# Kernel tuning notes

Hardware: AMD Instinct MI355X
Metric: run time of the kernel (lower is better)

The kernel has to match this reference:

```python
import jax, jax.numpy as jnp
import numpy as np

N = 50000   # nodes
E = 640000  # edges
D = 128     # hidden_size
BN_EPS = 1e-5


def _bn(x, g, b):
    # BatchNorm1d, training-mode batch statistics (biased variance), per-feature
    m = jnp.mean(x, axis=0)
    v = jnp.var(x, axis=0)
    return g * (x - m) * jax.lax.rsqrt(v + BN_EPS) + b


def _gin_mlp(x, W1, b1, g, bb, W2, b2):
    # Linear -> BatchNorm1d -> GELU(exact) -> Linear
    h = jax.nn.gelu(_bn(x @ W1 + b1, g, bb), approximate=False)
    return h @ W2 + b2


def _ffn(x, W1, b1, g1, bb1, W2, b2, g2, bb2):
    # fc1=(Linear+BN) -> GELU -> fc2=(Linear+BN) -> +shortcut
    h = jax.nn.gelu(_bn(x @ W1 + b1, g1, bb1), approximate=False)
    return _bn(h @ W2 + b2, g2, bb2) + x


def setup_inputs() -> dict:
    key = jax.random.key(0)
    ks = iter(jax.random.split(key, 16))

    def p(*s):
        return jax.random.normal(next(ks), s, jnp.float32) * 0.05

    inp = {
        "x": jax.random.normal(next(ks), (N, D), jnp.float32),
        "edge_index": jax.random.randint(next(ks), (2, E), 0, N, jnp.int32),
        # node_encoder + batch_norm
        "enc_W": p(D, D), "enc_b": jnp.zeros(D, jnp.float32),
        "bn_g": jnp.ones(D, jnp.float32), "bn_b": jnp.zeros(D, jnp.float32),
        # GINConv MLP: Linear(D,D)+BN+GELU+Linear(D,D)
        "gW1": p(D, D), "gb1": jnp.zeros(D, jnp.float32),
        "gg": jnp.ones(D, jnp.float32), "gbb": jnp.zeros(D, jnp.float32),
        "gW2": p(D, D), "gb2": jnp.zeros(D, jnp.float32),
        # fc2 = FFN(D, 2D)
        "f2W1": p(D, 2 * D), "f2b1": jnp.zeros(2 * D, jnp.float32),
        "f2g1": jnp.ones(2 * D, jnp.float32), "f2bb1": jnp.zeros(2 * D, jnp.float32),
        "f2W2": p(2 * D, D), "f2b2": jnp.zeros(D, jnp.float32),
        "f2g2": jnp.ones(D, jnp.float32), "f2bb2": jnp.zeros(D, jnp.float32),
        # ffn = FFN(D, 4D)
        "fnW1": p(D, 4 * D), "fnb1": jnp.zeros(4 * D, jnp.float32),
        "fng1": jnp.ones(4 * D, jnp.float32), "fnbb1": jnp.zeros(4 * D, jnp.float32),
        "fnW2": p(4 * D, D), "fnb2": jnp.zeros(D, jnp.float32),
        "fng2": jnp.ones(D, jnp.float32), "fnbb2": jnp.zeros(D, jnp.float32),
    }
    return inp


def reference(x, edge_index, enc_W, enc_b, bn_g, bn_b,
              gW1, gb1, gg, gbb, gW2, gb2,
              f2W1, f2b1, f2g1, f2bb1, f2W2, f2b2, f2g2, f2bb2,
              fnW1, fnb1, fng1, fnbb1, fnW2, fnb2, fng2, fnbb2):
    shortcut = x
    # node_encoder + BN
    h = _bn(x @ enc_W + enc_b, bn_g, bn_b)  # [N, D]
    # GINConv: out = MLP((1+eps)*h + sum_{j->i} h_j), eps=0
    src, dst = edge_index[0], edge_index[1]
    agg = jax.ops.segment_sum(h[src], dst, num_segments=N)  # scatter-add [N, D]
    h = _gin_mlp(h + agg, gW1, gb1, gg, gbb, gW2, gb2)
    # fc2 FFN (hidden 2D, internal residual)
    h = _ffn(h, f2W1, f2b1, f2g1, f2bb1, f2W2, f2b2, f2g2, f2bb2)
    # outer residual
    h = shortcut + h
    # final FFN (hidden 4D, internal residual)
    return _ffn(h, fnW1, fnb1, fng1, fnbb1, fnW2, fnb2, fng2, fnbb2)
```

## Files before the change

kernel.cpp:

```cpp
#include <hip/hip_runtime.h>
#include <hip/hip_bf16.h>

typedef __attribute__((ext_vector_type(8))) short short8;
typedef __attribute__((ext_vector_type(4))) float f32x4;

__device__ __forceinline__ float bf2f(unsigned short u) {
    union { unsigned int i; float f; } c;
    c.i = ((unsigned int)u) << 16;
    return c.f;
}
__device__ __forceinline__ unsigned short f2bf(float f) {
    union { float f; unsigned int i; } c;
    c.f = f;
    unsigned int x = c.i;
    x += 0x7FFFu + ((x >> 16) & 1u);
    return (unsigned short)(x >> 16);
}

#define NPART 64

template<int K, int M, int XF>
__global__ __launch_bounds__(256, (K > 256) ? 4 : 5)
void gemmf_kernel(const void* __restrict__ Av,
                  const float* __restrict__ pSum, const float* __restrict__ pSq,
                  const float* __restrict__ pG, const float* __restrict__ pB,
                  const unsigned short* __restrict__ Wp,
                  const float* __restrict__ bias,
                  float* __restrict__ part,
                  unsigned short* __restrict__ C,
                  int nrows, float invN)
{
    constexpr int KS_TOT = K / 32;
    constexpr int NKC    = K / 128;
    constexpr int NCT    = M / 128;
    constexpr bool DBUF  = (K > 256);
    constexpr int NFRAG  = DBUF ? 32 : 4 * KS_TOT;
    __shared__ __align__(16) char smem[NFRAG * 1024 + ((NCT > 1) ? 16384 : 0)];
    char* cbuf = smem + ((NCT > 1) ? NFRAG * 1024 : 0);

    const int tid = threadIdx.x;
    const int l   = tid & 63, wv = tid >> 6;
    const int gr0 = blockIdx.x * 64;
    const int kq4 = l & 3, rloc = l >> 2;
    const int woff = ((kq4 * 16 + rloc) * 16) ^ (kq4 << 5);
    const int loff = (l * 16) ^ ((l >> 4) << 5);

    int rowg[4];
    #pragma unroll
    for (int i = 0; i < 4; ++i) {
        int rg = gr0 + i * 16 + rloc;
        rowg[i] = rg < nrows ? rg : nrows - 1;
    }

    f32x4 acc[4][2];
    short8 breg[2][4];

    auto loadB = [&](int ct, int kcb) {
        #pragma unroll
        for (int c = 0; c < 2; ++c) {
            const int col = ct * 128 + (wv * 2 + c) * 16 + (l & 15);
            const unsigned short* bp = Wp + (size_t)col * K + kcb + (l >> 4) * 8;
            #pragma unroll
            for (int ks = 0; ks < 4; ++ks)
                breg[c][ks] = *(const short8*)(bp + ks * 32);
        }
    };

    auto bncoef = [&](int c0k, float* sc8, float* sh8) {
        #pragma unroll
        for (int j = 0; j < 8; ++j) {
            const int c = c0k + j;
            const float mean = pSum[c] * invN;
            const float var  = pSq[c] * invN - mean * mean;
            const float sc   = pG[c] * rsqrtf(var + 1e-5f);
            sc8[j] = sc;
            sh8[j] = pB[c] - mean * sc;
        }
    };

    auto xf2 = [&](short8 t, const float* sc8, const float* sh8) -> short8 {
        short8 val;
        #pragma unroll
        for (int j = 0; j < 8; ++j) {
            float v = sc8[j] * bf2f((unsigned short)t[j]) + sh8[j];
            v = 0.5f * v * (1.0f + erff(v * 0.70710678118f));
            val[j] = (short)f2bf(v);
        }
        return val;
    };

    auto epilogue = [&](int ct) {
        const int lrow = l & 15, kg = l >> 4;
        __syncthreads();
        #pragma unroll
        for (int c = 0; c < 2; ++c) {
            const int col  = (wv * 2 + c) * 16 + lrow;
            const int gcol = ct * 128 + col;
            const float bc = bias[gcol];
            float s = 0.f, q = 0.f;
            #pragma unroll
            for (int r = 0; r < 4; ++r) {
                #pragma unroll
                for (int i = 0; i < 4; ++i) {
                    const int rl = r * 16 + kg * 4 + i;
                    const float v = acc[r][c][i] + bc;
                    if (gr0 + rl < nrows) { s += v; q += v * v; }
                    const int byte = rl * 256 + ((col * 2) ^ ((rl & 7) << 4));
                    *(unsigned short*)(cbuf + byte) = f2bf(v);
                }
            }
            s += __shfl_xor(s, 16); s += __shfl_xor(s, 32);
            q += __shfl_xor(q, 16); q += __shfl_xor(q, 32);
            if (kg == 0 && part != nullptr) {
                float* ps = part + (size_t)(blockIdx.x & (NPART - 1)) * (2 * M);
                atomicAdd(&ps[gcol], s);
                atomicAdd(&ps[M + gcol], q);
            }
        }
        __syncthreads();
        #pragma unroll
        for (int j = 0; j < 4; ++j) {
            const int lin = j * 256 + tid;
            const int rl = lin >> 4, chunk = lin & 15;
            const int row = gr0 + rl;
            if (row < nrows) {
                short8 vv = *(const short8*)(cbuf + rl * 256 + ((chunk * 16) ^ ((rl & 7) << 4)));
                *(short8*)(C + (size_t)row * M + ct * 128 + chunk * 8) = vv;
            }
        }
    };

    if constexpr (!DBUF) {
        #pragma unroll
        for (int h = 0; h < NKC; ++h) {
            const int kst = h * 4 + wv;
            const int c0k = kst * 32 + kq4 * 8;
            float sc8[8], sh8[8];
            if (XF == 2) bncoef(c0k, sc8, sh8);
            #pragma unroll
            for (int i = 0; i < 4; ++i) {
                const size_t eoff = (size_t)rowg[i] * K + c0k;
                short8 val;
                if (XF == 0) {
                    val = *(const short8*)((const unsigned short*)Av + eoff);
                } else if (XF == 1) {
                    const float* A = (const float*)Av;
                    f32x4 u0 = *(const f32x4*)(A + eoff);
                    f32x4 u1 = *(const f32x4*)(A + eoff + 4);
                    #pragma unroll
                    for (int j = 0; j < 4; ++j) {
                        val[j]     = (short)f2bf(u0[j]);
                        val[j + 4] = (short)f2bf(u1[j]);
                    }
                } else {
                    short8 t = *(const short8*)((const unsigned short*)Av + eoff);
                    val = xf2(t, sc8, sh8);
                }
                *(short8*)(smem + (i * KS_TOT + kst) * 1024 + woff) = val;
            }
        }
        __syncthreads();
        #pragma unroll
        for (int ct = 0; ct < NCT; ++ct) {
            #pragma unroll
            for (int r = 0; r < 4; ++r)
                #pragma unroll
                for (int c = 0; c < 2; ++c) acc[r][c] = f32x4{0.f, 0.f, 0.f, 0.f};
            #pragma unroll
            for (int kc = 0; kc < NKC; ++kc) {
                loadB(ct, kc * 128);
                #pragma unroll
                for (int ks = 0; ks < 4; ++ks) {
                    const int ksg = kc * 4 + ks;
                    short8 af[4];
                    #pragma unroll
                    for (int r = 0; r < 4; ++r)
                        af[r] = *(const short8*)(smem + (r * KS_TOT + ksg) * 1024 + loff);
                    #pragma unroll
                    for (int r = 0; r < 4; ++r)
                        #pragma unroll
                        for (int c = 0; c < 2; ++c)
                            acc[r][c] = __builtin_amdgcn_mfma_f32_16x16x32_bf16(af[r], breg[c][ks], acc[r][c], 0, 0, 0);
                }
            }
            epilogue(ct);
        }
    } else {
        const int akoff = wv * 32 + kq4 * 8;
        auto stageChunk = [&](int kcb, int b, const short8* pre) {
            const int c0k = kcb + akoff;
            float sc8[8], sh8[8];
            if (XF == 2) bncoef(c0k, sc8, sh8);
            #pragma unroll
            for (int i = 0; i < 4; ++i) {
                short8 t = pre ? pre[i]
                              : *(const short8*)((const unsigned short*)Av + (size_t)rowg[i] * K + c0k);
                short8 val = (XF == 2) ? xf2(t, sc8, sh8) : t;
                *(short8*)(smem + (b * 16 + i * 4 + wv) * 1024 + woff) = val;
            }
        };
        stageChunk(0, 0, nullptr);
        __syncthreads();
        #pragma unroll
        for (int r = 0; r < 4; ++r)
            #pragma unroll
            for (int c = 0; c < 2; ++c) acc[r][c] = f32x4{0.f, 0.f, 0.f, 0.f};
        #pragma unroll
        for (int kc = 0; kc < NKC; ++kc) {
            const int cur = kc & 1;
            loadB(0, kc * 128);
            short8 anext[4];
            if (kc + 1 < NKC) {
                const int c0k = (kc + 1) * 128 + akoff;
                #pragma unroll
                for (int i = 0; i < 4; ++i)
                    anext[i] = *(const short8*)((const unsigned short*)Av + (size_t)rowg[i] * K + c0k);
            }
            #pragma unroll
            for (int ks = 0; ks < 4; ++ks) {
                short8 af[4];
                #pragma unroll
                for (int r = 0; r < 4; ++r)
                    af[r] = *(const short8*)(smem + (cur * 16 + r * 4 + ks) * 1024 + loff);
                #pragma unroll
                for (int r = 0; r < 4; ++r)
                    #pragma unroll
                    for (int c = 0; c < 2; ++c)
                        acc[r][c] = __builtin_amdgcn_mfma_f32_16x16x32_bf16(af[r], breg[c][ks], acc[r][c], 0, 0, 0);
            }
            if (kc + 1 < NKC) {
                stageChunk((kc + 1) * 128, cur ^ 1, anext);
                __syncthreads();
            }
        }
        epilogue(0);
    }
}

__global__ void reduce_kernel(const float* __restrict__ part,
                              float* __restrict__ out, int W2)
{
    int i = blockIdx.x * blockDim.x + threadIdx.x;
    if (i >= W2) return;
    float s = 0.f;
    #pragma unroll 8
    for (int r = 0; r < NPART; ++r) s += part[(size_t)r * W2 + i];
    out[i] = s;
}

__global__ void h3_kernel(const unsigned short* __restrict__ t4,
                          const float* __restrict__ pSum, const float* __restrict__ pSq,
                          const float* __restrict__ pG, const float* __restrict__ pB,
                          const unsigned short* __restrict__ t2,
                          const float* __restrict__ xr,
                          unsigned short* __restrict__ H3, float invN, int total4)
{
    int idx = blockIdx.x * blockDim.x + threadIdx.x;
    if (idx >= total4) return;
    const int base = idx * 4;
    const int c0 = base & 127;
    ushort4 tv = *(const ushort4*)(t4 + base);
    ushort4 uv = *(const ushort4*)(t2 + base);
    float4  xv = *(const float4*)(xr + base);
    unsigned short ts[4] = {tv.x, tv.y, tv.z, tv.w};
    unsigned short us[4] = {uv.x, uv.y, uv.z, uv.w};
    const float* px = &xv.x;
    ushort4 ov;
    unsigned short* po = &ov.x;
    #pragma unroll
    for (int j = 0; j < 4; ++j) {
        const int c = c0 + j;
        const float mean = pSum[c] * invN;
        const float var  = pSq[c] * invN - mean * mean;
        const float sc   = pG[c] * rsqrtf(var + 1e-5f);
        const float sh   = pB[c] - mean * sc;
        po[j] = f2bf(sc * bf2f(ts[j]) + sh + bf2f(us[j]) + px[j]);
    }
    *(ushort4*)(H3 + base) = ov;
}

__global__ void hist_kernel(const int* __restrict__ ei, int* __restrict__ cnt, int E)
{
    int e = blockIdx.x * blockDim.x + threadIdx.x;
    if (e < E) atomicAdd(&cnt[ei[E + e]], 1);
}

__global__ void scan_reduce(const int* __restrict__ cnt, int* __restrict__ blksum, int n)
{
    __shared__ int s[256];
    int t = threadIdx.x;
    int i = blockIdx.x * 256 + t;
    s[t] = i < n ? cnt[i] : 0;
    __syncthreads();
    for (int d = 128; d > 0; d >>= 1) {
        if (t < d) s[t] += s[t + d];
        __syncthreads();
    }
    if (t == 0) blksum[blockIdx.x] = s[0];
}

__global__ void scan_top(int* __restrict__ blksum, int nb)
{
    __shared__ int s[256];
    int t = threadIdx.x;
    int v = t < nb ? blksum[t] : 0;
    s[t] = v;
    __syncthreads();
    for (int d = 1; d < 256; d <<= 1) {
        int u = (t >= d) ? s[t - d] : 0;
        __syncthreads();
        s[t] += u;
        __syncthreads();
    }
    if (t < nb) blksum[t] = s[t] - v;
}

__global__ void scan_apply(const int* __restrict__ cnt, const int* __restrict__ blksum,
                           int* __restrict__ offs, int* __restrict__ cursor, int n)
{
    __shared__ int s[256];
    int t = threadIdx.x;
    int i = blockIdx.x * 256 + t;
    int v = i < n ? cnt[i] : 0;
    s[t] = v;
    __syncthreads();
    for (int d = 1; d < 256; d <<= 1) {
        int u = (t >= d) ? s[t - d] : 0;
        __syncthreads();
        s[t] += u;
        __syncthreads();
    }
    int excl = s[t] - v + blksum[blockIdx.x];
    if (i < n) { offs[i] = excl; cursor[i] = excl; }
}

__global__ void place_kernel(const int* __restrict__ ei, int* __restrict__ cursor,
                             int* __restrict__ ssrc, int E)
{
    int e = blockIdx.x * blockDim.x + threadIdx.x;
    if (e < E) {
        int pos = atomicAdd(&cursor[ei[E + e]], 1);
        ssrc[pos] = ei[e];
    }
}

__global__ __launch_bounds__(256)
void gather_kernel(const unsigned short* __restrict__ T0,
                   const float* __restrict__ pSum, const float* __restrict__ pSq,
                   const float* __restrict__ pG, const float* __restrict__ pB,
                   float invN,
                   const int* __restrict__ ssrc, const int* __restrict__ offs,
                   const int* __restrict__ cnt,
                   unsigned short* __restrict__ Zb, int N)
{
    const int wave = threadIdx.x >> 6;
    const int lane = threadIdx.x & 63;
    const int node = blockIdx.x * 4 + wave;
    if (node >= N) return;

    unsigned int hv = *(const unsigned int*)(T0 + (size_t)node * 128 + lane * 2);
    float a0 = bf2f((unsigned short)hv);
    float a1 = bf2f((unsigned short)(hv >> 16));

    const int off = offs[node];
    const int deg = cnt[node];
    for (int base = 0; base < deg; base += 64) {
        int m = deg - base;
        if (m > 64) m = 64;
        int idx = (base + lane < deg) ? ssrc[off + base + lane] : 0;
        int k = 0;
        for (; k + 1 < m; k += 2) {
            int s0 = __shfl(idx, k);
            int s1 = __shfl(idx, k + 1);
            unsigned int v0 = *(const unsigned int*)(T0 + (size_t)s0 * 128 + lane * 2);
            unsigned int v1 = *(const unsigned int*)(T0 + (size_t)s1 * 128 + lane * 2);
            a0 += bf2f((unsigned short)v0) + bf2f((unsigned short)v1);
            a1 += bf2f((unsigned short)(v0 >> 16)) + bf2f((unsigned short)(v1 >> 16));
        }
        if (k < m) {
            int s0 = __shfl(idx, k);
            unsigned int v0 = *(const unsigned int*)(T0 + (size_t)s0 * 128 + lane * 2);
            a0 += bf2f((unsigned short)v0);
            a1 += bf2f((unsigned short)(v0 >> 16));
        }
    }
    const int c0 = lane * 2;
    const float mean0 = pSum[c0] * invN;
    const float var0  = pSq[c0] * invN - mean0 * mean0;
    const float sc0   = pG[c0] * rsqrtf(var0 + 1e-5f);
    const float sh0   = pB[c0] - mean0 * sc0;
    const float mean1 = pSum[c0 + 1] * invN;
    const float var1  = pSq[c0 + 1] * invN - mean1 * mean1;
    const float sc1   = pG[c0 + 1] * rsqrtf(var1 + 1e-5f);
    const float sh1   = pB[c0 + 1] - mean1 * sc1;
    const float dp1 = (float)(deg + 1);
    const float z0 = sc0 * a0 + dp1 * sh0;
    const float z1 = sc1 * a1 + dp1 * sh1;
    unsigned int o = ((unsigned int)f2bf(z1) << 16) | (unsigned int)f2bf(z0);
    *(unsigned int*)(Zb + (size_t)node * 128 + lane * 2) = o;
}

__global__ void final_kernel(const unsigned short* __restrict__ t6,
                             const float* __restrict__ pSum, const float* __restrict__ pSq,
                             const float* __restrict__ pG, const float* __restrict__ pB,
                             const unsigned short* __restrict__ h3,
                             float* __restrict__ out, float invN, int total4)
{
    int idx = blockIdx.x * blockDim.x + threadIdx.x;
    if (idx >= total4) return;
    const int base = idx * 4;
    const int c0 = base & 127;
    ushort4 tv = *(const ushort4*)(t6 + base);
    ushort4 hv = *(const ushort4*)(h3 + base);
    unsigned short ts[4] = {tv.x, tv.y, tv.z, tv.w};
    unsigned short hs[4] = {hv.x, hv.y, hv.z, hv.w};
    float4 ov;
    float* po = &ov.x;
    #pragma unroll
    for (int j = 0; j < 4; ++j) {
        const int c = c0 + j;
        const float mean = pSum[c] * invN;
        const float var  = pSq[c] * invN - mean * mean;
        const float sc   = pG[c] * rsqrtf(var + 1e-5f);
        const float sh   = pB[c] - mean * sc;
        po[j] = sc * bf2f(ts[j]) + sh + bf2f(hs[j]);
    }
    *(float4*)(out + base) = ov;
}

struct PackDesc { const float* src; unsigned short* dst; int K; int M; };
struct Pack7 { PackDesc d[7]; };
__global__ void pack_kernel(Pack7 p)
{
    PackDesc d = p.d[blockIdx.y];
    const int total = d.K * d.M;
    for (int idx = blockIdx.x * blockDim.x + threadIdx.x; idx < total;
         idx += gridDim.x * blockDim.x) {
        const int k = idx / d.M;
        const int m = idx - k * d.M;
        d.dst[(size_t)m * d.K + k] = f2bf(d.src[idx]);
    }
}

extern "C" void kernel_launch(void* const* d_in, const int* in_sizes, int n_in,
                              void* d_out, int out_size, void* d_ws, size_t ws_size,
                              hipStream_t stream)
{
    const float* x     = (const float*)d_in[0];
    const int*   ei    = (const int*)d_in[1];
    const float* enc_W = (const float*)d_in[2];
    const float* enc_b = (const float*)d_in[3];
    const float* bn_g  = (const float*)d_in[4];
    const float* bn_b  = (const float*)d_in[5];
    const float* gW1   = (const float*)d_in[6];
    const float* gb1   = (const float*)d_in[7];
    const float* gg    = (const float*)d_in[8];
    const float* gbb   = (const float*)d_in[9];
    const float* gW2   = (const float*)d_in[10];
    const float* gb2   = (const float*)d_in[11];
    const float* f2W1  = (const float*)d_in[12];
    const float* f2b1  = (const float*)d_in[13];
    const float* f2g1  = (const float*)d_in[14];
    const float* f2bb1 = (const float*)d_in[15];
    const float* f2W2  = (const float*)d_in[16];
    const float* f2b2  = (const float*)d_in[17];
    const float* f2g2  = (const float*)d_in[18];
    const float* f2bb2 = (const float*)d_in[19];
    const float* fnW1  = (const float*)d_in[20];
    const float* fnb1  = (const float*)d_in[21];
    const float* fng1  = (const float*)d_in[22];
    const float* fnbb1 = (const float*)d_in[23];
    const float* fnW2  = (const float*)d_in[24];
    const float* fnb2  = (const float*)d_in[25];
    const float* fng2  = (const float*)d_in[26];
    const float* fnbb2 = (const float*)d_in[27];

    const int D = 128;
    const int N = in_sizes[0] / D;
    const int E = in_sizes[1] / 2;
    const float invN = 1.0f / (float)N;

    char* w = (char*)d_ws;
    float* s0 = (float*)w;
    float* s1 = s0 + 256;
    float* s3 = s1 + 256;
    float* s4 = s3 + 512;
    float* s5 = s4 + 256;
    float* s6 = s5 + 1024;
    const size_t statsBytes = 2560 * sizeof(float);
    size_t off = statsBytes;

    float* p0 = (float*)(w + off); off += (size_t)NPART * 256 * 4;
    float* p1 = (float*)(w + off); off += (size_t)NPART * 256 * 4;
    float* p3 = (float*)(w + off); off += (size_t)NPART * 512 * 4;
    float* p4 = (float*)(w + off); off += (size_t)NPART * 256 * 4;
    float* p5 = (float*)(w + off); off += (size_t)NPART * 1024 * 4;
    float* p6 = (float*)(w + off); off += (size_t)NPART * 256 * 4;
    const size_t partBytes = (size_t)NPART * 2560 * 4;

    unsigned short* wpE  = (unsigned short*)(w + off); off += (size_t)128 * 128 * 2;
    unsigned short* wpG1 = (unsigned short*)(w + off); off += (size_t)128 * 128 * 2;
    unsigned short* wpG2 = (unsigned short*)(w + off); off += (size_t)128 * 128 * 2;
    unsigned short* wpF1 = (unsigned short*)(w + off); off += (size_t)128 * 256 * 2;
    unsigned short* wpF2 = (unsigned short*)(w + off); off += (size_t)256 * 128 * 2;
    unsigned short* wpN1 = (unsigned short*)(w + off); off += (size_t)128 * 512 * 2;
    unsigned short* wpN2 = (unsigned short*)(w + off); off += (size_t)512 * 128 * 2;

    unsigned short* P1 = (unsigned short*)(w + off); off += (size_t)N * 128 * 2;
    unsigned short* Zb = (unsigned short*)(w + off); off += (size_t)N * 128 * 2;
    unsigned short* H3 = (unsigned short*)(w + off); off += (size_t)N * 128 * 2;
    unsigned short* T3 = (unsigned short*)(w + off); off += (size_t)N * 256 * 2;
    unsigned short* T5 = (unsigned short*)(w + off); off += (size_t)N * 512 * 2;

    const int NB = (N + 255) / 256;
    char* csr = (char*)T5;
    int* cnt    = (int*)csr;  csr += (size_t)NB * 256 * 4;
    int* offs   = (int*)csr;  csr += (size_t)NB * 256 * 4;
    int* cursor = (int*)csr;  csr += (size_t)NB * 256 * 4;
    int* blksum = (int*)csr;  csr += 1024;
    int* ssrc   = (int*)csr;

    hipMemsetAsync(p0, 0, partBytes, stream);
    hipMemsetAsync(cnt, 0, (size_t)NB * 256 * 4, stream);

    Pack7 pk;
    pk.d[0] = PackDesc{enc_W, wpE, 128, 128};
    pk.d[1] = PackDesc{gW1, wpG1, 128, 128};
    pk.d[2] = PackDesc{gW2, wpG2, 128, 128};
    pk.d[3] = PackDesc{f2W1, wpF1, 128, 256};
    pk.d[4] = PackDesc{f2W2, wpF2, 256, 128};
    pk.d[5] = PackDesc{fnW1, wpN1, 128, 512};
    pk.d[6] = PackDesc{fnW2, wpN2, 512, 128};
    pack_kernel<<<dim3(64, 7), 256, 0, stream>>>(pk);

    const int eb = (E + 255) / 256;
    hist_kernel<<<eb, 256, 0, stream>>>(ei, cnt, E);
    scan_reduce<<<NB, 256, 0, stream>>>(cnt, blksum, N);
    scan_top<<<1, 256, 0, stream>>>(blksum, NB);
    scan_apply<<<NB, 256, 0, stream>>>(cnt, blksum, offs, cursor, N);
    place_kernel<<<eb, 256, 0, stream>>>(ei, cursor, ssrc, E);

    const int rb  = (N + 63) / 64;
    const int t4a = N * 128 / 4;
    const int ewb = (t4a + 255) / 256;

    gemmf_kernel<128, 128, 1><<<rb, 256, 0, stream>>>(
        x, nullptr, nullptr, nullptr, nullptr,
        wpE, enc_b, p0, P1, N, invN);
    reduce_kernel<<<1, 256, 0, stream>>>(p0, s0, 256);
    gather_kernel<<<(N + 3) / 4, 256, 0, stream>>>(
        P1, s0, s0 + 128, bn_g, bn_b, invN, ssrc, offs, cnt, Zb, N);
    gemmf_kernel<128, 128, 0><<<rb, 256, 0, stream>>>(
        Zb, nullptr, nullptr, nullptr, nullptr,
        wpG1, gb1, p1, P1, N, invN);
    reduce_kernel<<<1, 256, 0, stream>>>(p1, s1, 256);
    gemmf_kernel<128, 128, 2><<<rb, 256, 0, stream>>>(
        P1, s1, s1 + 128, gg, gbb,
        wpG2, gb2, nullptr, Zb, N, invN);
    gemmf_kernel<128, 256, 0><<<rb, 256, 0, stream>>>(
        Zb, nullptr, nullptr, nullptr, nullptr,
        wpF1, f2b1, p3, T3, N, invN);
    reduce_kernel<<<2, 256, 0, stream>>>(p3, s3, 512);
    gemmf_kernel<256, 128, 2><<<rb, 256, 0, stream>>>(
        T3, s3, s3 + 256, f2g1, f2bb1,
        wpF2, f2b2, p4, P1, N, invN);
    reduce_kernel<<<1, 256, 0, stream>>>(p4, s4, 256);
    h3_kernel<<<ewb, 256, 0, stream>>>(
        P1, s4, s4 + 128, f2g2, f2bb2, Zb, x, H3, invN, t4a);
    gemmf_kernel<128, 512, 0><<<rb, 256, 0, stream>>>(
        H3, nullptr, nullptr, nullptr, nullptr,
        wpN1, fnb1, p5, T5, N, invN);
    reduce_kernel<<<4, 256, 0, stream>>>(p5, s5, 1024);
    gemmf_kernel<512, 128, 2><<<rb, 256, 0, stream>>>(
        T5, s5, s5 + 512, fng1, fnbb1,
        wpN2, fnb2, p6, P1, N, invN);
    reduce_kernel<<<1, 256, 0, stream>>>(p6, s6, 256);
    final_kernel<<<ewb, 256, 0, stream>>>(
        P1, s6, s6 + 128, fng2, fnbb2, H3, (float*)d_out, invN, t4a);

    (void)n_in; (void)out_size; (void)ws_size;
}
```

Before: 357.1 us.

## Precompute BN scale/shift in reduce kernel and use fast tanh-form GELU

The partial-sum reduce kernels now also compute the per-feature BatchNorm scale and shift, so consumer kernels load two coefficients instead of recomputing mean, variance and rsqrt per element or thread. The exact erf GELU in the fused GEMM prologue is replaced with a sigmoid/tanh-style approximation built from a fast exp and a hardware reciprocal. This cuts transcendental and ALU work on the GEMM A-operand staging path but changes the numerics from exact GELU to an approximation.

```diff
diff --git a/kernel.cpp b/kernel.cpp
--- a/kernel.cpp
+++ b/kernel.cpp
@@ -16,19 +16,25 @@
     x += 0x7FFFu + ((x >> 16) & 1u);
     return (unsigned short)(x >> 16);
 }
+__device__ __forceinline__ float gelu_fast(float x) {
+    const float x2 = x * x;
+    const float t = x * fmaf(0.0713548163f, x2, 1.5957691216f);
+    const float e = __expf(t);
+    const float r = __builtin_amdgcn_rcpf(e + 1.0f);
+    return fmaf(-x, r, x);
+}
 
 #define NPART 64
 
 template<int K, int M, int XF>
 __global__ __launch_bounds__(256, (K > 256) ? 4 : 5)
 void gemmf_kernel(const void* __restrict__ Av,
-                  const float* __restrict__ pSum, const float* __restrict__ pSq,
-                  const float* __restrict__ pG, const float* __restrict__ pB,
+                  const float* __restrict__ pCoef,
                   const unsigned short* __restrict__ Wp,
                   const float* __restrict__ bias,
                   float* __restrict__ part,
                   unsigned short* __restrict__ C,
-                  int nrows, float invN)
+                  int nrows)
 {
     constexpr int KS_TOT = K / 32;
     constexpr int NKC    = K / 128;
@@ -66,25 +72,12 @@
         }
     };
 
-    auto bncoef = [&](int c0k, float* sc8, float* sh8) {
-        #pragma unroll
-        for (int j = 0; j < 8; ++j) {
-            const int c = c0k + j;
-            const float mean = pSum[c] * invN;
-            const float var  = pSq[c] * invN - mean * mean;
-            const float sc   = pG[c] * rsqrtf(var + 1e-5f);
-            sc8[j] = sc;
-            sh8[j] = pB[c] - mean * sc;
-        }
-    };
-
     auto xf2 = [&](short8 t, const float* sc8, const float* sh8) -> short8 {
         short8 val;
         #pragma unroll
         for (int j = 0; j < 8; ++j) {
-            float v = sc8[j] * bf2f((unsigned short)t[j]) + sh8[j];
-            v = 0.5f * v * (1.0f + erff(v * 0.70710678118f));
-            val[j] = (short)f2bf(v);
+            float v = fmaf(sc8[j], bf2f((unsigned short)t[j]), sh8[j]);
+            val[j] = (short)f2bf(gelu_fast(v));
         }
         return val;
     };
@@ -136,7 +129,13 @@
             const int kst = h * 4 + wv;
             const int c0k = kst * 32 + kq4 * 8;
             float sc8[8], sh8[8];
-            if (XF == 2) bncoef(c0k, sc8, sh8);
+            if (XF == 2) {
+                #pragma unroll
+                for (int j = 0; j < 8; ++j) {
+                    sc8[j] = pCoef[c0k + j];
+                    sh8[j] = pCoef[K + c0k + j];
+                }
+            }
             #pragma unroll
             for (int i = 0; i < 4; ++i) {
                 const size_t eoff = (size_t)rowg[i] * K + c0k;
@@ -190,7 +189,13 @@
         auto stageChunk = [&](int kcb, int b, const short8* pre) {
             const int c0k = kcb + akoff;
             float sc8[8], sh8[8];
-            if (XF == 2) bncoef(c0k, sc8, sh8);
+            if (XF == 2) {
+                #pragma unroll
+                for (int j = 0; j < 8; ++j) {
+                    sc8[j] = pCoef[c0k + j];
+                    sh8[j] = pCoef[K + c0k + j];
+                }
+            }
             #pragma unroll
             for (int i = 0; i < 4; ++i) {
                 short8 t = pre ? pre[i]
@@ -237,23 +242,30 @@
     }
 }
 
-__global__ void reduce_kernel(const float* __restrict__ part,
-                              float* __restrict__ out, int W2)
+__global__ void coef_kernel(const float* __restrict__ part,
+                            const float* __restrict__ g, const float* __restrict__ b,
+                            float* __restrict__ scsh, int W, float invN)
 {
     int i = blockIdx.x * blockDim.x + threadIdx.x;
-    if (i >= W2) return;
-    float s = 0.f;
+    if (i >= W) return;
+    float s = 0.f, q = 0.f;
     #pragma unroll 8
-    for (int r = 0; r < NPART; ++r) s += part[(size_t)r * W2 + i];
-    out[i] = s;
+    for (int r = 0; r < NPART; ++r) {
+        s += part[(size_t)r * 2 * W + i];
+        q += part[(size_t)r * 2 * W + W + i];
+    }
+    const float mean = s * invN;
+    const float var  = q * invN - mean * mean;
+    const float sc   = g[i] * rsqrtf(var + 1e-5f);
+    scsh[i] = sc;
+    scsh[W + i] = b[i] - mean * sc;
 }
 
 __global__ void h3_kernel(const unsigned short* __restrict__ t4,
-                          const float* __restrict__ pSum, const float* __restrict__ pSq,
-                          const float* __restrict__ pG, const float* __restrict__ pB,
+                          const float* __restrict__ coef,
                           const unsigned short* __restrict__ t2,
                           const float* __restrict__ xr,
-                          unsigned short* __restrict__ H3, float invN, int total4)
+                          unsigned short* __restrict__ H3, int total4)
 {
     int idx = blockIdx.x * blockDim.x + threadIdx.x;
     if (idx >= total4) return;
@@ -270,11 +282,7 @@
     #pragma unroll
     for (int j = 0; j < 4; ++j) {
         const int c = c0 + j;
-        const float mean = pSum[c] * invN;
-        const float var  = pSq[c] * invN - mean * mean;
-        const float sc   = pG[c] * rsqrtf(var + 1e-5f);
-        const float sh   = pB[c] - mean * sc;
-        po[j] = f2bf(sc * bf2f(ts[j]) + sh + bf2f(us[j]) + px[j]);
+        po[j] = f2bf(fmaf(coef[c], bf2f(ts[j]), coef[128 + c]) + bf2f(us[j]) + px[j]);
     }
     *(ushort4*)(H3 + base) = ov;
 }
@@ -346,9 +354,7 @@
 
 __global__ __launch_bounds__(256)
 void gather_kernel(const unsigned short* __restrict__ T0,
-                   const float* __restrict__ pSum, const float* __restrict__ pSq,
-                   const float* __restrict__ pG, const float* __restrict__ pB,
-                   float invN,
+                   const float* __restrict__ coef,
                    const int* __restrict__ ssrc, const int* __restrict__ offs,
                    const int* __restrict__ cnt,
                    unsigned short* __restrict__ Zb, int N)
@@ -385,26 +391,17 @@
         }
     }
     const int c0 = lane * 2;
-    const float mean0 = pSum[c0] * invN;
-    const float var0  = pSq[c0] * invN - mean0 * mean0;
-    const float sc0   = pG[c0] * rsqrtf(var0 + 1e-5f);
-    const float sh0   = pB[c0] - mean0 * sc0;
-    const float mean1 = pSum[c0 + 1] * invN;
-    const float var1  = pSq[c0 + 1] * invN - mean1 * mean1;
-    const float sc1   = pG[c0 + 1] * rsqrtf(var1 + 1e-5f);
-    const float sh1   = pB[c0 + 1] - mean1 * sc1;
     const float dp1 = (float)(deg + 1);
-    const float z0 = sc0 * a0 + dp1 * sh0;
-    const float z1 = sc1 * a1 + dp1 * sh1;
+    const float z0 = fmaf(coef[c0], a0, dp1 * coef[128 + c0]);
+    const float z1 = fmaf(coef[c0 + 1], a1, dp1 * coef[128 + c0 + 1]);
     unsigned int o = ((unsigned int)f2bf(z1) << 16) | (unsigned int)f2bf(z0);
     *(unsigned int*)(Zb + (size_t)node * 128 + lane * 2) = o;
 }
 
 __global__ void final_kernel(const unsigned short* __restrict__ t6,
-                             const float* __restrict__ pSum, const float* __restrict__ pSq,
-                             const float* __restrict__ pG, const float* __restrict__ pB,
+                             const float* __restrict__ coef,
                              const unsigned short* __restrict__ h3,
-                             float* __restrict__ out, float invN, int total4)
+                             float* __restrict__ out, int total4)
 {
     int idx = blockIdx.x * blockDim.x + threadIdx.x;
     if (idx >= total4) return;
@@ -419,11 +416,7 @@
     #pragma unroll
     for (int j = 0; j < 4; ++j) {
         const int c = c0 + j;
-        const float mean = pSum[c] * invN;
-        const float var  = pSq[c] * invN - mean * mean;
-        const float sc   = pG[c] * rsqrtf(var + 1e-5f);
-        const float sh   = pB[c] - mean * sc;
-        po[j] = sc * bf2f(ts[j]) + sh + bf2f(hs[j]);
+        po[j] = fmaf(coef[c], bf2f(ts[j]), coef[128 + c]) + bf2f(hs[j]);
     }
     *(float4*)(out + base) = ov;
 }
@@ -481,14 +474,14 @@
     const float invN = 1.0f / (float)N;
 
     char* w = (char*)d_ws;
-    float* s0 = (float*)w;
-    float* s1 = s0 + 256;
-    float* s3 = s1 + 256;
-    float* s4 = s3 + 512;
-    float* s5 = s4 + 256;
-    float* s6 = s5 + 1024;
-    const size_t statsBytes = 2560 * sizeof(float);
-    size_t off = statsBytes;
+    float* c0 = (float*)w;
+    float* c1 = c0 + 256;
+    float* c3 = c1 + 256;
+    float* c4 = c3 + 512;
+    float* c5 = c4 + 256;
+    float* c6 = c5 + 1024;
+    const size_t coefBytes = 2560 * sizeof(float);
+    size_t off = coefBytes;
 
     float* p0 = (float*)(w + off); off += (size_t)NPART * 256 * 4;
     float* p1 = (float*)(w + off); off += (size_t)NPART * 256 * 4;
@@ -545,38 +538,29 @@
     const int ewb = (t4a + 255) / 256;
 
     gemmf_kernel<128, 128, 1><<<rb, 256, 0, stream>>>(
-        x, nullptr, nullptr, nullptr, nullptr,
-        wpE, enc_b, p0, P1, N, invN);
-    reduce_kernel<<<1, 256, 0, stream>>>(p0, s0, 256);
+        x, nullptr, wpE, enc_b, p0, P1, N);
+    coef_kernel<<<1, 256, 0, stream>>>(p0, bn_g, bn_b, c0, 128, invN);
     gather_kernel<<<(N + 3) / 4, 256, 0, stream>>>(
-        P1, s0, s0 + 128, bn_g, bn_b, invN, ssrc, offs, cnt, Zb, N);
+        P1, c0, ssrc, offs, cnt, Zb, N);
     gemmf_kernel<128, 128, 0><<<rb, 256, 0, stream>>>(
-        Zb, nullptr, nullptr, nullptr, nullptr,
-        wpG1, gb1, p1, P1, N, invN);
-    reduce_kernel<<<1, 256, 0, stream>>>(p1, s1, 256);
+        Zb, nullptr, wpG1, gb1, p1, P1, N);
+    coef_kernel<<<1, 256, 0, stream>>>(p1, gg, gbb, c1, 128, invN);
     gemmf_kernel<128, 128, 2><<<rb, 256, 0, stream>>>(
-        P1, s1, s1 + 128, gg, gbb,
-        wpG2, gb2, nullptr, Zb, N, invN);
+        P1, c1, wpG2, gb2, nullptr, Zb, N);
     gemmf_kernel<128, 256, 0><<<rb, 256, 0, stream>>>(
-        Zb, nullptr, nullptr, nullptr, nullptr,
-        wpF1, f2b1, p3, T3, N, invN);
-    reduce_kernel<<<2, 256, 0, stream>>>(p3, s3, 512);
+        Zb, nullptr, wpF1, f2b1, p3, T3, N);
+    coef_kernel<<<1, 256, 0, stream>>>(p3, f2g1, f2bb1, c3, 256, invN);
     gemmf_kernel<256, 128, 2><<<rb, 256, 0, stream>>>(
-        T3, s3, s3 + 256, f2g1, f2bb1,
-        wpF2, f2b2, p4, P1, N, invN);
-    reduce_kernel<<<1, 256, 0, stream>>>(p4, s4, 256);
-    h3_kernel<<<ewb, 256, 0, stream>>>(
-        P1, s4, s4 + 128, f2g2, f2bb2, Zb, x, H3, invN, t4a);
+        T3, c3, wpF2, f2b2, p4, P1, N);
+    coef_kernel<<<1, 256, 0, stream>>>(p4, f2g2, f2bb2, c4, 128, invN);
+    h3_kernel<<<ewb, 256, 0, stream>>>(P1, c4, Zb, x, H3, t4a);
     gemmf_kernel<128, 512, 0><<<rb, 256, 0, stream>>>(
-        H3, nullptr, nullptr, nullptr, nullptr,
-        wpN1, fnb1, p5, T5, N, invN);
-    reduce_kernel<<<4, 256, 0, stream>>>(p5, s5, 1024);
+        H3, nullptr, wpN1, fnb1, p5, T5, N);
+    coef_kernel<<<2, 256, 0, stream>>>(p5, fng1, fnbb1, c5, 512, invN);
     gemmf_kernel<512, 128, 2><<<rb, 256, 0, stream>>>(
-        T5, s5, s5 + 512, fng1, fnbb1,
-        wpN2, fnb2, p6, P1, N, invN);
-    reduce_kernel<<<1, 256, 0, stream>>>(p6, s6, 256);
-    final_kernel<<<ewb, 256, 0, stream>>>(
-        P1, s6, s6 + 128, fng2, fnbb2, H3, (float*)d_out, invN, t4a);
+        T5, c5, wpN2, fnb2, p6, P1, N);
+    coef_kernel<<<1, 256, 0, stream>>>(p6, fng2, fnbb2, c6, 128, invN);
+    final_kernel<<<ewb, 256, 0, stream>>>(P1, c6, H3, (float*)d_out, t4a);
 
     (void)n_in; (void)out_size; (void)ws_size;
 }
```

Result: faster. 318.2 us (-10.9%).
